# Optimization experiments

Hardware: AMD Instinct MI355X
Metric: run time of the kernel (lower is better)

## Reference

```python
import jax, jax.numpy as jnp
import numpy as np

NUM_ANCHORS_LIST = [6400, 1600, 400]  # 640x640 input, strides 8/16/32
TOPK = 9
NUM_CLASSES = 80
EPS = 1e-9


def _make_anchors():
    boxes = []
    for fs, stride in [(80, 8), (40, 16), (20, 32)]:
        c = (np.arange(fs, dtype=np.float32) + 0.5) * stride
        cy, cx = np.meshgrid(c, c, indexing='ij')
        cx = cx.reshape(-1); cy = cy.reshape(-1)
        half = 2.5 * stride  # ATSS-style anchor: 5*stride square
        boxes.append(np.stack([cx - half, cy - half, cx + half, cy + half], axis=-1))
    return jnp.asarray(np.concatenate(boxes, axis=0))  # [8400, 4]


def setup_inputs() -> dict:
    key = jax.random.key(0)
    k1, k2, k3, k4 = jax.random.split(key, 4)
    B, M = 32, 64
    anchor_bboxes = _make_anchors()  # [A,4]
    cxy = jax.random.uniform(k1, (B, M, 2), minval=40.0, maxval=600.0)
    wh = jax.random.uniform(k2, (B, M, 2), minval=10.0, maxval=200.0)
    gt_bboxes = jnp.concatenate([cxy - wh / 2, cxy + wh / 2], axis=-1)  # [B,M,4]
    gt_labels = jax.random.randint(k3, (B, M), 0, NUM_CLASSES)  # int
    pad_gt_mask = jnp.ones((B, M, 1), dtype=jnp.float32)
    pred_bboxes = anchor_bboxes[None] + jax.random.normal(k4, (B, anchor_bboxes.shape[0], 4)) * 4.0
    return {
        'anchor_bboxes': anchor_bboxes,
        'gt_labels': gt_labels,
        'gt_bboxes': gt_bboxes,
        'pad_gt_mask': pad_gt_mask,
        'pred_bboxes': pred_bboxes,
        'bg_index': NUM_CLASSES,
    }


def _bbox_center(b):
    return jnp.stack([(b[..., 0] + b[..., 2]) * 0.5, (b[..., 1] + b[..., 3]) * 0.5], axis=-1)


def _iou(b1, b2):
    # b1 [..., N, 1, 4] vs b2 [..., 1, A, 4] -> [..., N, A]
    x1y1 = jnp.maximum(b1[..., 0:2], b2[..., 0:2])
    x2y2 = jnp.minimum(b1[..., 2:4], b2[..., 2:4])
    overlap = jnp.prod(jnp.maximum(x2y2 - x1y1, 0.0), axis=-1)
    a1 = jnp.prod(jnp.maximum(b1[..., 2:4] - b1[..., 0:2], 0.0), axis=-1)
    a2 = jnp.prod(jnp.maximum(b2[..., 2:4] - b2[..., 0:2], 0.0), axis=-1)
    return overlap / (a1 + a2 - overlap + EPS)


def _check_inside(points, bboxes):
    # points [A,2], bboxes [B,M,4] -> [B,M,A] float mask
    x = points[None, None, :, 0]
    y = points[None, None, :, 1]
    xmin, ymin, xmax, ymax = [bboxes[..., i:i + 1] for i in range(4)]
    ltrb_min = jnp.minimum(jnp.minimum(x - xmin, y - ymin), jnp.minimum(xmax - x, ymax - y))
    return (ltrb_min > EPS).astype(bboxes.dtype)


def _atss_forward(anchor_bboxes, gt_labels, gt_bboxes, pad_gt_mask, pred_bboxes, bg_index):
    B, M, _ = gt_bboxes.shape
    A = anchor_bboxes.shape[0]
    # pairwise IoU [B,M,A]
    ious = _iou(gt_bboxes[:, :, None, :], anchor_bboxes[None, None, :, :])
    gt_centers = _bbox_center(gt_bboxes)          # [B,M,2]
    anchor_centers = _bbox_center(anchor_bboxes)  # [A,2]
    dists = jnp.linalg.norm(gt_centers[:, :, None, :] - anchor_centers[None, None, :, :], axis=-1)  # [B,M,A]

    # per-level topk (smallest distance) + pyramid index offsets
    is_in_topk_list, topk_idx_list = [], []
    start = 0
    for n in NUM_ANCHORS_LIST:
        d = dists[..., start:start + n]
        _, idx = jax.lax.top_k(-d, TOPK)  # [B,M,TOPK], smallest distances
        topk_idx_list.append(idx + start)
        oh = jax.nn.one_hot(idx, n, dtype=dists.dtype).sum(axis=-2) * pad_gt_mask
        is_in_topk_list.append(oh)
        start += n
    is_in_topk = jnp.concatenate(is_in_topk_list, axis=-1)  # [B,M,A]
    topk_idxs = jnp.concatenate(topk_idx_list, axis=-1)     # [B,M,L*TOPK]

    iou_candidates = ious * is_in_topk
    thr = jnp.take_along_axis(iou_candidates, topk_idxs, axis=-1)  # [B,M,27]
    thr_v = thr.mean(axis=-1, keepdims=True) + thr.std(axis=-1, ddof=1, keepdims=True)  # torch.std is unbiased
    is_in_topk = jnp.where(iou_candidates > thr_v, is_in_topk, 0.0)

    is_in_gts = _check_inside(anchor_centers, gt_bboxes)
    mask_positive = is_in_topk * is_in_gts * pad_gt_mask  # [B,M,A]
    mps = mask_positive.sum(axis=-2)                      # [B,A]

    # resolve anchors matched to multiple gts by max IoU (identity when none)
    mask_multi = mps[:, None, :] > 1                       # [B,1,A] broadcast over M
    is_max_iou = jax.nn.one_hot(jnp.argmax(ious, axis=-2), M, dtype=ious.dtype).transpose(0, 2, 1)
    mask_positive = jnp.where(mask_multi, is_max_iou, mask_positive)
    mps = mask_positive.sum(axis=-2)

    assigned_gt_index = jnp.argmax(mask_positive, axis=-2)  # [B,A]
    assigned_labels = jnp.take_along_axis(gt_labels, assigned_gt_index, axis=-1)
    assigned_labels = jnp.where(mps > 0, assigned_labels, bg_index)
    assigned_bboxes = jnp.take_along_axis(gt_bboxes, assigned_gt_index[..., None], axis=1)  # [B,A,4]

    scores = jax.nn.one_hot(assigned_labels, NUM_CLASSES + 1, dtype=jnp.float32)
    keep = jnp.asarray([i for i in range(NUM_CLASSES + 1) if i != bg_index])
    scores = scores[..., keep]  # [B,A,NUM_CLASSES]

    # pred_bboxes branch: modulate scores by max IoU(gt, pred) over positives
    pious = _iou(gt_bboxes[:, :, None, :], pred_bboxes[:, None, :, :]) * mask_positive  # [B,M,A]
    scores = scores * pious.max(axis=-2)[..., None]
    return assigned_labels, assigned_bboxes, scores


def reference(anchor_bboxes, gt_labels, gt_bboxes, pad_gt_mask, pred_bboxes, bg_index):
    return _atss_forward(anchor_bboxes, gt_labels, gt_bboxes, pad_gt_mask, pred_bboxes, bg_index)
```

## Files before the change

kernel.cpp:

```cpp
#include <hip/hip_runtime.h>
#include <cstdint>
#include <cstddef>

#define TOPK 9
#define NCLS 80
#define EPSF 1e-9f

__device__ __forceinline__ float iou_f(float4 b1, float4 b2) {
    float x1 = fmaxf(b1.x, b2.x), y1 = fmaxf(b1.y, b2.y);
    float x2 = fminf(b1.z, b2.z), y2 = fminf(b1.w, b2.w);
    float ov = fmaxf(x2 - x1, 0.f) * fmaxf(y2 - y1, 0.f);
    float a1 = fmaxf(b1.z - b1.x, 0.f) * fmaxf(b1.w - b1.y, 0.f);
    float a2 = fmaxf(b2.z - b2.x, 0.f) * fmaxf(b2.w - b2.y, 0.f);
    return ov / (a1 + a2 - ov + EPSF);
}

__global__ __launch_bounds__(256) void zero_mask_kernel(unsigned long long* p, int n) {
    int t = blockIdx.x * blockDim.x + threadIdx.x;
    if (t < n) p[t] = 0ull;
}

__global__ __launch_bounds__(64) void atss_topk_kernel(
    const float* __restrict__ anchors,
    const float* __restrict__ gt_bboxes,
    const float* __restrict__ pad_mask,
    unsigned long long* __restrict__ pos_mask,
    int M, int A) {
    const int bm = blockIdx.x;
    const int b = bm / M;
    const int m = bm - b * M;
    const int lane = threadIdx.x;

    const float4 g = ((const float4*)gt_bboxes)[bm];
    const float gcx = (g.x + g.z) * 0.5f;
    const float gcy = (g.y + g.w) * 0.5f;

    __shared__ unsigned idx27[32];
    __shared__ float    iou27[32];

    const int fsL[3]  = {80, 40, 20};
    const int strL[3] = {8, 16, 32};
    const int stL[3]  = {0, 6400, 8000};

    const int wx = lane & 7;
    const int wy = lane >> 3;

    for (int lvl = 0; lvl < 3; ++lvl) {
        const int fs = fsL[lvl];
        const float s = (float)strL[lvl];
        const int st = stL[lvl];

        int fx = (int)floorf(gcx / s - 0.5f);
        int fy = (int)floorf(gcy / s - 0.5f);
        int ix0 = min(max(fx - 3, 0), fs - 8);
        int iy0 = min(max(fy - 3, 0), fs - 8);

        int gi = st + (iy0 + wy) * fs + (ix0 + wx);
        float4 a = ((const float4*)anchors)[gi];
        float ddx = (a.x + a.z) * 0.5f - gcx;
        float ddy = (a.y + a.w) * 0.5f - gcy;
        float d = sqrtf(ddx * ddx + ddy * ddy);
        unsigned long long v =
            ((unsigned long long)__float_as_uint(d) << 32) | (unsigned)gi;

#pragma unroll
        for (int r = 0; r < TOPK; ++r) {
            unsigned long long mn = v;
#pragma unroll
            for (int sft = 32; sft >= 1; sft >>= 1) {
                unsigned long long o = __shfl_xor(mn, sft, 64);
                mn = (o < mn) ? o : mn;
            }
            if (lane == 0) idx27[lvl * TOPK + r] = (unsigned)mn;
            if (v == mn) v = ~0ull;
        }
    }
    __syncthreads();

    if (lane < 27) {
        float4 a = ((const float4*)anchors)[idx27[lane]];
        iou27[lane] = iou_f(g, a);
    }
    __syncthreads();

    float sum = 0.f;
    for (int k = 0; k < 27; ++k) sum += iou27[k];
    float mean = sum * (1.0f / 27.0f);
    float var = 0.f;
    for (int k = 0; k < 27; ++k) {
        float d = iou27[k] - mean;
        var += d * d;
    }
    float thr = mean + sqrtf(var * (1.0f / 26.0f));

    float pad = pad_mask[bm];
    if (lane < 27 && pad != 0.f) {
        if (iou27[lane] > thr) {
            unsigned ai = idx27[lane];
            float4 a = ((const float4*)anchors)[ai];
            float acx = (a.x + a.z) * 0.5f;
            float acy = (a.y + a.w) * 0.5f;
            float lt = fminf(fminf(acx - g.x, acy - g.y),
                             fminf(g.z - acx, g.w - acy));
            if (lt > EPSF) {
                atomicOr(&pos_mask[(size_t)b * A + ai], 1ull << m);
            }
        }
    }
}

__global__ __launch_bounds__(256) void atss_assign_kernel(
    const float* __restrict__ anchors,
    const int*   __restrict__ gt_labels,
    const float* __restrict__ gt_bboxes,
    const float* __restrict__ pred,
    const int*   __restrict__ bg_ptr,
    const unsigned long long* __restrict__ pos_mask,
    float* __restrict__ out_labels,
    float* __restrict__ out_bboxes,
    float* __restrict__ piou_ws,
    int M, int A, int BA) {
    int t = blockIdx.x * blockDim.x + threadIdx.x;
    if (t >= BA) return;
    int b = t / A;
    int a = t - b * A;

    unsigned long long mask = pos_mask[t];
    int mps = __popcll(mask);

    int gt = 0;
    if (mps == 1) {
        gt = __builtin_ctzll(mask);
    } else if (mps > 1) {
        float4 an = ((const float4*)anchors)[a];
        float best = -1.f;
        for (int mm = 0; mm < M; ++mm) {
            float v = iou_f(((const float4*)gt_bboxes)[b * M + mm], an);
            if (v > best) { best = v; gt = mm; }
        }
    }

    float4 gbox = ((const float4*)gt_bboxes)[b * M + gt];
    int label = (mps > 0) ? gt_labels[b * M + gt] : bg_ptr[0];

    out_labels[t] = (float)label;
    ((float4*)out_bboxes)[t] = gbox;

    float pi = 0.f;
    if (mps > 0) {
        float4 p = ((const float4*)pred)[t];
        pi = iou_f(gbox, p);
    }
    piou_ws[t] = pi;
}

__global__ __launch_bounds__(256) void atss_scores_kernel(
    const float* __restrict__ out_labels,
    const float* __restrict__ piou_ws,
    float* __restrict__ scores,
    int total4) {
    int t = blockIdx.x * blockDim.x + threadIdx.x;
    if (t >= total4) return;
    int anchor = t / (NCLS / 4);
    int c0 = (t - anchor * (NCLS / 4)) * 4;
    int label = (int)out_labels[anchor];
    float pi = piou_ws[anchor];
    float4 v;
    v.x = (c0 + 0 == label) ? pi : 0.f;
    v.y = (c0 + 1 == label) ? pi : 0.f;
    v.z = (c0 + 2 == label) ? pi : 0.f;
    v.w = (c0 + 3 == label) ? pi : 0.f;
    ((float4*)scores)[t] = v;
}

extern "C" void kernel_launch(void* const* d_in, const int* in_sizes, int n_in,
                              void* d_out, int out_size, void* d_ws, size_t ws_size,
                              hipStream_t stream) {
    const float* anchors   = (const float*)d_in[0];
    const int*   gt_labels = (const int*)d_in[1];
    const float* gt_bboxes = (const float*)d_in[2];
    const float* pad_mask  = (const float*)d_in[3];
    const float* pred      = (const float*)d_in[4];
    const int*   bg_ptr    = (const int*)d_in[5];

    const int A  = in_sizes[0] / 4;
    const int BM = in_sizes[1];
    const int M  = 64;
    const int B  = BM / M;
    const int BA = B * A;

    float* out_labels = (float*)d_out;
    float* out_bboxes = out_labels + (size_t)BA;
    float* scores     = out_bboxes + (size_t)BA * 4;

    unsigned long long* pos_mask = (unsigned long long*)d_ws;
    float* piou_ws = (float*)((char*)d_ws + (size_t)BA * sizeof(unsigned long long));

    zero_mask_kernel<<<(BA + 255) / 256, 256, 0, stream>>>(pos_mask, BA);
    atss_topk_kernel<<<BM, 64, 0, stream>>>(anchors, gt_bboxes, pad_mask,
                                            pos_mask, M, A);
    atss_assign_kernel<<<(BA + 255) / 256, 256, 0, stream>>>(
        anchors, gt_labels, gt_bboxes, pred, bg_ptr, pos_mask,
        out_labels, out_bboxes, piou_ws, M, A, BA);
    const int total4 = BA * (NCLS / 4);
    atss_scores_kernel<<<(total4 + 255) / 256, 256, 0, stream>>>(
        out_labels, piou_ws, scores, total4);
}
```

Measured before the change: 144.7 us.

## Parallelize top-k across pyramid levels with rank sort and use nontemporal score stores

The top-k kernel now runs one wavefront per pyramid level in a 192-thread block instead of looping over the three levels in one wave. The 9-round shuffle-min selection becomes a single rank computation: each lane counts smaller keys across the wave and writes itself if its rank is below 9, which relies on the keys being unique. The scores kernel writes its large one-hot output with nontemporal stores so the data does not pollute the cache. Together these shorten the serial dependency chain per GT box and lower cache pressure from the score writes.

```diff
diff --git a/kernel.cpp b/kernel.cpp
--- a/kernel.cpp
+++ b/kernel.cpp
@@ -5,6 +5,8 @@
 #define TOPK 9
 #define NCLS 80
 #define EPSF 1e-9f
+
+typedef float f4v __attribute__((ext_vector_type(4)));
 
 __device__ __forceinline__ float iou_f(float4 b1, float4 b2) {
     float x1 = fmaxf(b1.x, b2.x), y1 = fmaxf(b1.y, b2.y);
@@ -20,7 +22,7 @@
     if (t < n) p[t] = 0ull;
 }
 
-__global__ __launch_bounds__(64) void atss_topk_kernel(
+__global__ __launch_bounds__(192) void atss_topk_kernel(
     const float* __restrict__ anchors,
     const float* __restrict__ gt_bboxes,
     const float* __restrict__ pad_mask,
@@ -29,7 +31,8 @@
     const int bm = blockIdx.x;
     const int b = bm / M;
     const int m = bm - b * M;
-    const int lane = threadIdx.x;
+    const int lane = threadIdx.x & 63;
+    const int w = threadIdx.x >> 6;
 
     const float4 g = ((const float4*)gt_bboxes)[bm];
     const float gcx = (g.x + g.z) * 0.5f;
@@ -42,64 +45,58 @@
     const int strL[3] = {8, 16, 32};
     const int stL[3]  = {0, 6400, 8000};
 
+    const int fs = fsL[w];
+    const float s = (float)strL[w];
+    const int st = stL[w];
+
+    int fx = (int)floorf(gcx / s - 0.5f);
+    int fy = (int)floorf(gcy / s - 0.5f);
+    int ix0 = min(max(fx - 3, 0), fs - 8);
+    int iy0 = min(max(fy - 3, 0), fs - 8);
+
     const int wx = lane & 7;
     const int wy = lane >> 3;
-
-    for (int lvl = 0; lvl < 3; ++lvl) {
-        const int fs = fsL[lvl];
-        const float s = (float)strL[lvl];
-        const int st = stL[lvl];
-
-        int fx = (int)floorf(gcx / s - 0.5f);
-        int fy = (int)floorf(gcy / s - 0.5f);
-        int ix0 = min(max(fx - 3, 0), fs - 8);
-        int iy0 = min(max(fy - 3, 0), fs - 8);
-
-        int gi = st + (iy0 + wy) * fs + (ix0 + wx);
-        float4 a = ((const float4*)anchors)[gi];
-        float ddx = (a.x + a.z) * 0.5f - gcx;
-        float ddy = (a.y + a.w) * 0.5f - gcy;
-        float d = sqrtf(ddx * ddx + ddy * ddy);
-        unsigned long long v =
-            ((unsigned long long)__float_as_uint(d) << 32) | (unsigned)gi;
-
+    int gi = st + (iy0 + wy) * fs + (ix0 + wx);
+    float4 a = ((const float4*)anchors)[gi];
+    float ddx = (a.x + a.z) * 0.5f - gcx;
+    float ddy = (a.y + a.w) * 0.5f - gcy;
+    float d = sqrtf(ddx * ddx + ddy * ddy);
+    unsigned long long key =
+        ((unsigned long long)__float_as_uint(d) << 32) | (unsigned)gi;
+
+    int rank = 0;
 #pragma unroll
-        for (int r = 0; r < TOPK; ++r) {
-            unsigned long long mn = v;
-#pragma unroll
-            for (int sft = 32; sft >= 1; sft >>= 1) {
-                unsigned long long o = __shfl_xor(mn, sft, 64);
-                mn = (o < mn) ? o : mn;
-            }
-            if (lane == 0) idx27[lvl * TOPK + r] = (unsigned)mn;
-            if (v == mn) v = ~0ull;
+    for (int j = 0; j < 64; ++j) {
+        unsigned long long o = __shfl(key, j, 64);
+        rank += (o < key) ? 1 : 0;
+    }
+    if (rank < TOPK)
+        idx27[w * TOPK + rank] = (unsigned)(key & 0xFFFFFFFFu);
+    __syncthreads();
+
+    if (threadIdx.x < 27) {
+        float4 ca = ((const float4*)anchors)[idx27[threadIdx.x]];
+        iou27[threadIdx.x] = iou_f(g, ca);
+    }
+    __syncthreads();
+
+    if (threadIdx.x < 27) {
+        float sum = 0.f;
+        for (int k = 0; k < 27; ++k) sum += iou27[k];
+        float mean = sum * (1.0f / 27.0f);
+        float var = 0.f;
+        for (int k = 0; k < 27; ++k) {
+            float dd = iou27[k] - mean;
+            var += dd * dd;
         }
-    }
-    __syncthreads();
-
-    if (lane < 27) {
-        float4 a = ((const float4*)anchors)[idx27[lane]];
-        iou27[lane] = iou_f(g, a);
-    }
-    __syncthreads();
-
-    float sum = 0.f;
-    for (int k = 0; k < 27; ++k) sum += iou27[k];
-    float mean = sum * (1.0f / 27.0f);
-    float var = 0.f;
-    for (int k = 0; k < 27; ++k) {
-        float d = iou27[k] - mean;
-        var += d * d;
-    }
-    float thr = mean + sqrtf(var * (1.0f / 26.0f));
-
-    float pad = pad_mask[bm];
-    if (lane < 27 && pad != 0.f) {
-        if (iou27[lane] > thr) {
-            unsigned ai = idx27[lane];
-            float4 a = ((const float4*)anchors)[ai];
-            float acx = (a.x + a.z) * 0.5f;
-            float acy = (a.y + a.w) * 0.5f;
+        float thr = mean + sqrtf(var * (1.0f / 26.0f));
+
+        float pad = pad_mask[bm];
+        if (pad != 0.f && iou27[threadIdx.x] > thr) {
+            unsigned ai = idx27[threadIdx.x];
+            float4 ca = ((const float4*)anchors)[ai];
+            float acx = (ca.x + ca.z) * 0.5f;
+            float acy = (ca.y + ca.w) * 0.5f;
             float lt = fminf(fminf(acx - g.x, acy - g.y),
                              fminf(g.z - acx, g.w - acy));
             if (lt > EPSF) {
@@ -165,12 +162,12 @@
     int c0 = (t - anchor * (NCLS / 4)) * 4;
     int label = (int)out_labels[anchor];
     float pi = piou_ws[anchor];
-    float4 v;
+    f4v v;
     v.x = (c0 + 0 == label) ? pi : 0.f;
     v.y = (c0 + 1 == label) ? pi : 0.f;
     v.z = (c0 + 2 == label) ? pi : 0.f;
     v.w = (c0 + 3 == label) ? pi : 0.f;
-    ((float4*)scores)[t] = v;
+    __builtin_nontemporal_store(v, (f4v*)scores + t);
 }
 
 extern "C" void kernel_launch(void* const* d_in, const int* in_sizes, int n_in,
@@ -197,8 +194,8 @@
     float* piou_ws = (float*)((char*)d_ws + (size_t)BA * sizeof(unsigned long long));
 
     zero_mask_kernel<<<(BA + 255) / 256, 256, 0, stream>>>(pos_mask, BA);
-    atss_topk_kernel<<<BM, 64, 0, stream>>>(anchors, gt_bboxes, pad_mask,
-                                            pos_mask, M, A);
+    atss_topk_kernel<<<BM, 192, 0, stream>>>(anchors, gt_bboxes, pad_mask,
+                                             pos_mask, M, A);
     atss_assign_kernel<<<(BA + 255) / 256, 256, 0, stream>>>(
         anchors, gt_labels, gt_bboxes, pred, bg_ptr, pos_mask,
         out_labels, out_bboxes, piou_ws, M, A, BA);
```

New measurement: 144.5 us. Within noise of the previous version (-0.1%).
